# Kernel optimization log

Measured on AMD Instinct MI355X. Metric: run time of the kernel, lower is better.

Reference implementation:

```python
import jax, jax.numpy as jnp
import numpy as np

B, S, D = 4, 2048, 1024
H, HD = 16, 64

def setup_inputs() -> dict:
    key = jax.random.key(0)
    ks = jax.random.split(key, 5)
    scale = 1.0 / np.sqrt(D)
    return {
        "x": jax.random.normal(ks[0], (B, S, D), dtype=jnp.float32),
        "Wq": jax.random.normal(ks[1], (D, D), dtype=jnp.float32) * scale,
        "Wk": jax.random.normal(ks[2], (D, D), dtype=jnp.float32) * scale,
        "Wv": jax.random.normal(ks[3], (D, D), dtype=jnp.float32) * scale,
        "Wo": jax.random.normal(ks[4], (D, D), dtype=jnp.float32) * scale,
        "bo": jnp.zeros((D,), dtype=jnp.float32),
    }

def reference(x, Wq, Wk, Wv, Wo, bo):
    batch, tokens, _ = x.shape
    # Linear weights applied as x @ W^T to match torch nn.Linear; here W is [out,in] equiv square
    q = (x @ Wq).reshape(batch, tokens, H, HD).transpose(0, 2, 1, 3)  # [B,H,S,HD]
    k = (x @ Wk).reshape(batch, tokens, H, HD).transpose(0, 2, 1, 3)
    v = (x @ Wv).reshape(batch, tokens, H, HD).transpose(0, 2, 1, 3)
    scores = jnp.einsum('bhqd,bhkd->bhqk', q, k) / jnp.sqrt(jnp.float32(HD))
    causal = jnp.tril(jnp.ones((tokens, tokens), dtype=bool))  # True = keep
    scores = jnp.where(causal[None, None], scores, -jnp.inf)
    attn = jax.nn.softmax(scores, axis=-1)  # dropout is identity (eval / rate 0)
    ctx = jnp.einsum('bhqk,bhkd->bhqd', attn, v)
    ctx = ctx.transpose(0, 2, 1, 3).reshape(batch, tokens, D)
    return ctx @ Wo + bo
```

## Files before the change

kernel.cpp:

```cpp
#include <hip/hip_runtime.h>
#include <math.h>
#include <stdint.h>

constexpr int kB = 4;
constexpr int kS = 2048;
constexpr int kD = 1024;
constexpr int kH = 16;
constexpr int kHD = 64;

typedef __bf16 bf16;
typedef __attribute__((ext_vector_type(4))) __bf16 bf16x4;
typedef __attribute__((ext_vector_type(8))) __bf16 bf16x8;
typedef __attribute__((ext_vector_type(4))) float f32x4;

__device__ __forceinline__ f32x4 mfma16x16x32(bf16x8 a, bf16x8 b, f32x4 c) {
    return __builtin_amdgcn_mfma_f32_16x16x32_bf16(a, b, c, 0, 0, 0);
}

#if __has_builtin(__builtin_amdgcn_exp2f)
#define EXP2F(x) __builtin_amdgcn_exp2f(x)
#else
#define EXP2F(x) exp2f(x)
#endif

__device__ __forceinline__ void load_lds16(const bf16* g, bf16* lds) {
    __builtin_amdgcn_global_load_lds(
        (const __attribute__((address_space(1))) void*)g,
        (__attribute__((address_space(3))) void*)lds, 16, 0, 0);
}

__global__ __launch_bounds__(256) void prep_x(const float* __restrict__ x,
                                              bf16* __restrict__ xb) {
    size_t i = ((size_t)blockIdx.x * 256 + threadIdx.x) * 8;
    float4 f0 = *(const float4*)(x + i);
    float4 f1 = *(const float4*)(x + i + 4);
    bf16x8 v;
    v[0] = (bf16)f0.x; v[1] = (bf16)f0.y; v[2] = (bf16)f0.z; v[3] = (bf16)f0.w;
    v[4] = (bf16)f1.x; v[5] = (bf16)f1.y; v[6] = (bf16)f1.z; v[7] = (bf16)f1.w;
    *(bf16x8*)(xb + i) = v;
}

__global__ __launch_bounds__(256) void prep_w(const float* __restrict__ Wq,
                                              const float* __restrict__ Wk,
                                              const float* __restrict__ Wv,
                                              const float* __restrict__ Wo,
                                              bf16* __restrict__ Wt) {
    __shared__ bf16 t[64 * 72];
    const int z = blockIdx.z;
    const float* W = (z == 0) ? Wq : (z == 1) ? Wk : (z == 2) ? Wv : Wo;
    const float scale = (z == 0) ? 0.18033688011112042f : 1.0f;
    const int k0 = blockIdx.x * 64, n0 = blockIdx.y * 64;
    const int tid = threadIdx.x;
    for (int p = 0; p < 16; ++p) {
        int idx = tid + p * 256;
        int r = idx >> 6, c = idx & 63;
        t[r * 72 + c] = (bf16)(W[(size_t)(k0 + r) * kD + n0 + c] * scale);
    }
    __syncthreads();
    for (int p = 0; p < 16; ++p) {
        int idx = tid + p * 256;
        int r = idx >> 6, c = idx & 63;
        Wt[(size_t)(z * 1024 + n0 + r) * kD + k0 + c] = t[c * 72 + r];
    }
}

__global__ __launch_bounds__(256) void qkv_gemm(
    const bf16* __restrict__ xb, const bf16* __restrict__ Wt,
    bf16* __restrict__ qo, bf16* __restrict__ ko, bf16* __restrict__ vto)
{
    __shared__ bf16 As[128 * 32];
    __shared__ bf16 Bs[128 * 32];

    const int tid  = threadIdx.x;
    const int wave = tid >> 6;
    const int lane = tid & 63;
    const int quad = lane >> 4;
    const int lr   = lane & 15;
    const int wm   = wave >> 1, wn = wave & 1;

    const int m0 = blockIdx.x * 128;
    const int n0 = blockIdx.y * 128;

    const int sr = tid >> 2, sc = tid & 3;

    f32x4 acc[4][4];
#pragma unroll
    for (int i = 0; i < 4; ++i)
#pragma unroll
        for (int nt = 0; nt < 4; ++nt) acc[i][nt] = f32x4{0.f, 0.f, 0.f, 0.f};

    for (int k0 = 0; k0 < kD; k0 += 32) {
        __syncthreads();
#pragma unroll
        for (int p = 0; p < 2; ++p) {
            int r = p * 64 + sr;
            load_lds16(&xb[(size_t)(m0 + r) * kD + k0 + sc * 8],
                       &As[(p * 256 + wave * 64) * 8]);
            load_lds16(&Wt[(size_t)(n0 + r) * kD + k0 + sc * 8],
                       &Bs[(p * 256 + wave * 64) * 8]);
        }
        __syncthreads();
        bf16x8 a[4], b[4];
#pragma unroll
        for (int i = 0; i < 4; ++i)
            a[i] = *(const bf16x8*)&As[(wm * 64 + i * 16 + lr) * 32 + quad * 8];
#pragma unroll
        for (int nt = 0; nt < 4; ++nt)
            b[nt] = *(const bf16x8*)&Bs[(wn * 64 + nt * 16 + lr) * 32 + quad * 8];
#pragma unroll
        for (int i = 0; i < 4; ++i)
#pragma unroll
            for (int nt = 0; nt < 4; ++nt)
                acc[i][nt] = mfma16x16x32(a[i], b[nt], acc[i][nt]);
    }

    const int w_idx = n0 >> 10;
    if (w_idx < 2) {
        bf16* dst = (w_idx == 0) ? qo : ko;
#pragma unroll
        for (int i = 0; i < 4; ++i)
#pragma unroll
            for (int nt = 0; nt < 4; ++nt) {
                int n   = n0 + wn * 64 + nt * 16 + lr;
                int col = n & 1023;
#pragma unroll
                for (int j = 0; j < 4; ++j) {
                    int m = m0 + wm * 64 + i * 16 + quad * 4 + j;
                    dst[(size_t)m * kD + col] = (bf16)acc[i][nt][j];
                }
            }
    } else {
#pragma unroll
        for (int i = 0; i < 4; ++i)
#pragma unroll
            for (int nt = 0; nt < 4; ++nt) {
                int n   = n0 + wn * 64 + nt * 16 + lr;
                int col = n & 1023, h = col >> 6, hd = col & 63;
                int mb  = m0 + wm * 64 + i * 16 + quad * 4;
                int b = mb >> 11, s = mb & 2047;
                bf16x4 pk;
#pragma unroll
                for (int j = 0; j < 4; ++j) pk[j] = (bf16)acc[i][nt][j];
                *(bf16x4*)&vto[((size_t)(b * kH + h) * kHD + hd) * kS + s] = pk;
            }
    }
}

__global__ __launch_bounds__(256, 3) void attn(
    const bf16* __restrict__ q, const bf16* __restrict__ k,
    const bf16* __restrict__ vt, bf16* __restrict__ ctx)
{
    __shared__ bf16 Ks[2][64 * 64];
    __shared__ bf16 Vs[2][64 * 64];
    __shared__ bf16 Pl[4][16 * 72];

    const int tid  = threadIdx.x;
    const int wave = tid >> 6;
    const int lane = tid & 63;
    const int quad = lane >> 4;
    const int lr   = lane & 15;

    const int bh = blockIdx.x;
    const int qb = gridDim.y - 1 - blockIdx.y;
    const int b  = bh >> 4;
    const int h  = bh & 15;

    const bf16* qb_p = q  + (size_t)b * kS * kD + h * kHD;
    const bf16* kb_p = k  + (size_t)b * kS * kD + h * kHD;
    const bf16* vt_p = vt + (size_t)bh * kHD * kS;

    const int T    = qb + 1;
    const int base = qb * 64 + wave * 16;

    const int grow   = lane >> 3;
    const int gchunk = ((lane & 7) ^ (grow & 7)) * 8;

    bf16x8 ones;
#pragma unroll
    for (int i = 0; i < 8; ++i) ones[i] = (bf16)1.0f;

    bf16x8 aq[2];
#pragma unroll
    for (int kk = 0; kk < 2; ++kk)
        aq[kk] = *(const bf16x8*)&qb_p[(size_t)(base + lr) * kD + kk * 32 + quad * 8];

    f32x4 o[4];
    f32x4 lacc = f32x4{0.f, 0.f, 0.f, 0.f};
#pragma unroll
    for (int nt = 0; nt < 4; ++nt) o[nt] = f32x4{0.f, 0.f, 0.f, 0.f};

    bf16* Pw = &Pl[wave][0];

    if (wave == 0) {
#pragma unroll
        for (int i = 0; i < 8; ++i)
            load_lds16(kb_p + (size_t)(i * 8 + grow) * kD + gchunk, &Ks[0][i * 512]);
    } else if (wave == 1) {
#pragma unroll
        for (int i = 0; i < 8; ++i)
            load_lds16(vt_p + (size_t)(i * 8 + grow) * kS + gchunk, &Vs[0][i * 512]);
    }
    __syncthreads();

#pragma unroll 1
    for (int kt = 0; kt < T; ++kt) {
        const int k0  = kt * 64;
        const int buf = kt & 1;

        if (kt + 1 < T) {
            const int nk0 = k0 + 64;
            if (wave == 0) {
#pragma unroll
                for (int i = 0; i < 8; ++i)
                    load_lds16(kb_p + (size_t)(nk0 + i * 8 + grow) * kD + gchunk,
                               &Ks[buf ^ 1][i * 512]);
            } else if (wave == 1) {
#pragma unroll
                for (int i = 0; i < 8; ++i)
                    load_lds16(vt_p + (size_t)(i * 8 + grow) * kS + nk0 + gchunk,
                               &Vs[buf ^ 1][i * 512]);
            }
        }

        bf16x8 kf[4][2], vf[4][2];
#pragma unroll
        for (int nt = 0; nt < 4; ++nt)
#pragma unroll
            for (int kk = 0; kk < 2; ++kk) {
                const int sw = ((kk * 4 + quad) ^ (lr & 7)) << 3;
                kf[nt][kk] = *(const bf16x8*)&Ks[buf][(nt * 16 + lr) * 64 + sw];
                vf[nt][kk] = *(const bf16x8*)&Vs[buf][(nt * 16 + lr) * 64 + sw];
            }

        f32x4 sg[4];
        __builtin_amdgcn_s_setprio(1);
#pragma unroll
        for (int nt = 0; nt < 4; ++nt) {
            sg[nt] = mfma16x16x32(kf[nt][0], aq[0], f32x4{0.f, 0.f, 0.f, 0.f});
            sg[nt] = mfma16x16x32(kf[nt][1], aq[1], sg[nt]);
        }
        __builtin_amdgcn_s_setprio(0);

        if (kt == T - 1) {
            const int qg = base + lr;
#pragma unroll
            for (int nt = 0; nt < 4; ++nt) {
                bf16x4 pk;
#pragma unroll
                for (int j = 0; j < 4; ++j) {
                    float s = sg[nt][j];
                    s = (k0 + nt * 16 + quad * 4 + j > qg) ? -3.0e38f : s;
                    pk[j] = (bf16)EXP2F(s);
                }
                *(bf16x4*)&Pw[lr * 72 + nt * 16 + quad * 4] = pk;
            }
        } else {
#pragma unroll
            for (int nt = 0; nt < 4; ++nt) {
                bf16x4 pk;
#pragma unroll
                for (int j = 0; j < 4; ++j) pk[j] = (bf16)EXP2F(sg[nt][j]);
                *(bf16x4*)&Pw[lr * 72 + nt * 16 + quad * 4] = pk;
            }
        }

        __builtin_amdgcn_s_setprio(1);
#pragma unroll
        for (int kk = 0; kk < 2; ++kk) {
            bf16x8 pa = *(const bf16x8*)&Pw[lr * 72 + kk * 32 + quad * 8];
            lacc = mfma16x16x32(pa, ones, lacc);
#pragma unroll
            for (int nt = 0; nt < 4; ++nt)
                o[nt] = mfma16x16x32(pa, vf[nt][kk], o[nt]);
        }
        __builtin_amdgcn_s_setprio(0);

        __syncthreads();
    }

    float inv[4];
#pragma unroll
    for (int j = 0; j < 4; ++j) inv[j] = 1.0f / lacc[j];
#pragma unroll
    for (int nt = 0; nt < 4; ++nt) {
        int hd = nt * 16 + lr;
#pragma unroll
        for (int j = 0; j < 4; ++j) {
            int qg = base + quad * 4 + j;
            ctx[((size_t)(b * kS + qg)) * kD + h * kHD + hd] = (bf16)(o[nt][j] * inv[j]);
        }
    }
}

__global__ __launch_bounds__(256) void out_gemm(
    const bf16* __restrict__ ctxb, const bf16* __restrict__ Wto,
    const float* __restrict__ bo, float* __restrict__ out)
{
    __shared__ bf16 As[128 * 32];
    __shared__ bf16 Bs[128 * 32];

    const int tid  = threadIdx.x;
    const int wave = tid >> 6;
    const int lane = tid & 63;
    const int quad = lane >> 4;
    const int lr   = lane & 15;
    const int wm   = wave >> 1, wn = wave & 1;

    const int m0 = blockIdx.x * 128;
    const int n0 = blockIdx.y * 128;

    const int sr = tid >> 2, sc = tid & 3;

    f32x4 acc[4][4];
#pragma unroll
    for (int i = 0; i < 4; ++i)
#pragma unroll
        for (int nt = 0; nt < 4; ++nt) acc[i][nt] = f32x4{0.f, 0.f, 0.f, 0.f};

    for (int k0 = 0; k0 < kD; k0 += 32) {
        __syncthreads();
#pragma unroll
        for (int p = 0; p < 2; ++p) {
            int r = p * 64 + sr;
            load_lds16(&ctxb[(size_t)(m0 + r) * kD + k0 + sc * 8],
                       &As[(p * 256 + wave * 64) * 8]);
            load_lds16(&Wto[(size_t)(n0 + r) * kD + k0 + sc * 8],
                       &Bs[(p * 256 + wave * 64) * 8]);
        }
        __syncthreads();
        bf16x8 a[4], b[4];
#pragma unroll
        for (int i = 0; i < 4; ++i)
            a[i] = *(const bf16x8*)&As[(wm * 64 + i * 16 + lr) * 32 + quad * 8];
#pragma unroll
        for (int nt = 0; nt < 4; ++nt)
            b[nt] = *(const bf16x8*)&Bs[(wn * 64 + nt * 16 + lr) * 32 + quad * 8];
#pragma unroll
        for (int i = 0; i < 4; ++i)
#pragma unroll
            for (int nt = 0; nt < 4; ++nt)
                acc[i][nt] = mfma16x16x32(a[i], b[nt], acc[i][nt]);
    }

#pragma unroll
    for (int nt = 0; nt < 4; ++nt) {
        int n = n0 + wn * 64 + nt * 16 + lr;
        float bias = bo[n];
#pragma unroll
        for (int i = 0; i < 4; ++i)
#pragma unroll
            for (int j = 0; j < 4; ++j) {
                int m = m0 + wm * 64 + i * 16 + quad * 4 + j;
                out[(size_t)m * kD + n] = acc[i][nt][j] + bias;
            }
    }
}

extern "C" void kernel_launch(void* const* d_in, const int* in_sizes, int n_in,
                              void* d_out, int out_size, void* d_ws, size_t ws_size,
                              hipStream_t stream) {
    const float* x  = (const float*)d_in[0];
    const float* Wq = (const float*)d_in[1];
    const float* Wk = (const float*)d_in[2];
    const float* Wv = (const float*)d_in[3];
    const float* Wo = (const float*)d_in[4];
    const float* bo = (const float*)d_in[5];
    float* out = (float*)d_out;

    const size_t n_x   = (size_t)kB * kS * kD;
    const size_t n_w   = (size_t)4 * kD * kD;
    const size_t n_mat = (size_t)kB * kH * kS * kHD;

    bf16* xb  = (bf16*)d_ws;
    bf16* Wt  = xb + n_x;
    bf16* Qm  = Wt + n_w;
    bf16* Km  = Qm + n_mat;
    bf16* Vt  = Km + n_mat;
    bf16* ctx = xb;

    prep_x<<<dim3((int)(n_x / (256 * 8))), dim3(256), 0, stream>>>(x, xb);
    prep_w<<<dim3(16, 16, 4), dim3(256), 0, stream>>>(Wq, Wk, Wv, Wo, Wt);
    qkv_gemm<<<dim3(8192 / 128, 3072 / 128), dim3(256), 0, stream>>>(xb, Wt, Qm, Km, Vt);
    attn<<<dim3(kB * kH, 32), dim3(256), 0, stream>>>(Qm, Km, Vt, ctx);
    out_gemm<<<dim3(8192 / 128, 1024 / 128), dim3(256), 0, stream>>>(
        ctx, Wt + (size_t)3 * kD * kD, bo, out);
}
```

Baseline: 239.9 us.

## Double-buffer LDS tiles in QKV and output GEMMs with prefetch and setprio

Both projection GEMMs now hold two LDS buffers per operand. The next K-slice is issued as a direct global-to-LDS load while the current slice's MFMAs run, and the loop drops from two barriers per iteration to one. The MFMA block is wrapped in s_setprio to favour matrix issue. This doubles LDS use per block, which may lower occupancy, and correctness relies on the vmcnt wait that the single barrier implies for the async LDS loads.

```diff
diff --git a/kernel.cpp b/kernel.cpp
--- a/kernel.cpp
+++ b/kernel.cpp
@@ -68,8 +68,8 @@
     const bf16* __restrict__ xb, const bf16* __restrict__ Wt,
     bf16* __restrict__ qo, bf16* __restrict__ ko, bf16* __restrict__ vto)
 {
-    __shared__ bf16 As[128 * 32];
-    __shared__ bf16 Bs[128 * 32];
+    __shared__ bf16 As[2][128 * 32];
+    __shared__ bf16 Bs[2][128 * 32];
 
     const int tid  = threadIdx.x;
     const int wave = tid >> 6;
@@ -89,29 +89,44 @@
 #pragma unroll
         for (int nt = 0; nt < 4; ++nt) acc[i][nt] = f32x4{0.f, 0.f, 0.f, 0.f};
 
+#pragma unroll
+    for (int p = 0; p < 2; ++p) {
+        int r = p * 64 + sr;
+        load_lds16(&xb[(size_t)(m0 + r) * kD + sc * 8], &As[0][(p * 256 + wave * 64) * 8]);
+        load_lds16(&Wt[(size_t)(n0 + r) * kD + sc * 8], &Bs[0][(p * 256 + wave * 64) * 8]);
+    }
+    __syncthreads();
+
+    int buf = 0;
     for (int k0 = 0; k0 < kD; k0 += 32) {
-        __syncthreads();
-#pragma unroll
-        for (int p = 0; p < 2; ++p) {
-            int r = p * 64 + sr;
-            load_lds16(&xb[(size_t)(m0 + r) * kD + k0 + sc * 8],
-                       &As[(p * 256 + wave * 64) * 8]);
-            load_lds16(&Wt[(size_t)(n0 + r) * kD + k0 + sc * 8],
-                       &Bs[(p * 256 + wave * 64) * 8]);
-        }
-        __syncthreads();
+        if (k0 + 32 < kD) {
+#pragma unroll
+            for (int p = 0; p < 2; ++p) {
+                int r = p * 64 + sr;
+                load_lds16(&xb[(size_t)(m0 + r) * kD + k0 + 32 + sc * 8],
+                           &As[buf ^ 1][(p * 256 + wave * 64) * 8]);
+                load_lds16(&Wt[(size_t)(n0 + r) * kD + k0 + 32 + sc * 8],
+                           &Bs[buf ^ 1][(p * 256 + wave * 64) * 8]);
+            }
+        }
+
         bf16x8 a[4], b[4];
 #pragma unroll
         for (int i = 0; i < 4; ++i)
-            a[i] = *(const bf16x8*)&As[(wm * 64 + i * 16 + lr) * 32 + quad * 8];
+            a[i] = *(const bf16x8*)&As[buf][(wm * 64 + i * 16 + lr) * 32 + quad * 8];
 #pragma unroll
         for (int nt = 0; nt < 4; ++nt)
-            b[nt] = *(const bf16x8*)&Bs[(wn * 64 + nt * 16 + lr) * 32 + quad * 8];
+            b[nt] = *(const bf16x8*)&Bs[buf][(wn * 64 + nt * 16 + lr) * 32 + quad * 8];
+        __builtin_amdgcn_s_setprio(1);
 #pragma unroll
         for (int i = 0; i < 4; ++i)
 #pragma unroll
             for (int nt = 0; nt < 4; ++nt)
                 acc[i][nt] = mfma16x16x32(a[i], b[nt], acc[i][nt]);
+        __builtin_amdgcn_s_setprio(0);
+
+        __syncthreads();
+        buf ^= 1;
     }
 
     const int w_idx = n0 >> 10;
@@ -296,8 +311,8 @@
     const bf16* __restrict__ ctxb, const bf16* __restrict__ Wto,
     const float* __restrict__ bo, float* __restrict__ out)
 {
-    __shared__ bf16 As[128 * 32];
-    __shared__ bf16 Bs[128 * 32];
+    __shared__ bf16 As[2][128 * 32];
+    __shared__ bf16 Bs[2][128 * 32];
 
     const int tid  = threadIdx.x;
     const int wave = tid >> 6;
@@ -317,29 +332,44 @@
 #pragma unroll
         for (int nt = 0; nt < 4; ++nt) acc[i][nt] = f32x4{0.f, 0.f, 0.f, 0.f};
 
+#pragma unroll
+    for (int p = 0; p < 2; ++p) {
+        int r = p * 64 + sr;
+        load_lds16(&ctxb[(size_t)(m0 + r) * kD + sc * 8], &As[0][(p * 256 + wave * 64) * 8]);
+        load_lds16(&Wto[(size_t)(n0 + r) * kD + sc * 8], &Bs[0][(p * 256 + wave * 64) * 8]);
+    }
+    __syncthreads();
+
+    int buf = 0;
     for (int k0 = 0; k0 < kD; k0 += 32) {
-        __syncthreads();
-#pragma unroll
-        for (int p = 0; p < 2; ++p) {
-            int r = p * 64 + sr;
-            load_lds16(&ctxb[(size_t)(m0 + r) * kD + k0 + sc * 8],
-                       &As[(p * 256 + wave * 64) * 8]);
-            load_lds16(&Wto[(size_t)(n0 + r) * kD + k0 + sc * 8],
-                       &Bs[(p * 256 + wave * 64) * 8]);
-        }
-        __syncthreads();
+        if (k0 + 32 < kD) {
+#pragma unroll
+            for (int p = 0; p < 2; ++p) {
+                int r = p * 64 + sr;
+                load_lds16(&ctxb[(size_t)(m0 + r) * kD + k0 + 32 + sc * 8],
+                           &As[buf ^ 1][(p * 256 + wave * 64) * 8]);
+                load_lds16(&Wto[(size_t)(n0 + r) * kD + k0 + 32 + sc * 8],
+                           &Bs[buf ^ 1][(p * 256 + wave * 64) * 8]);
+            }
+        }
+
         bf16x8 a[4], b[4];
 #pragma unroll
         for (int i = 0; i < 4; ++i)
-            a[i] = *(const bf16x8*)&As[(wm * 64 + i * 16 + lr) * 32 + quad * 8];
+            a[i] = *(const bf16x8*)&As[buf][(wm * 64 + i * 16 + lr) * 32 + quad * 8];
 #pragma unroll
         for (int nt = 0; nt < 4; ++nt)
-            b[nt] = *(const bf16x8*)&Bs[(wn * 64 + nt * 16 + lr) * 32 + quad * 8];
+            b[nt] = *(const bf16x8*)&Bs[buf][(wn * 64 + nt * 16 + lr) * 32 + quad * 8];
+        __builtin_amdgcn_s_setprio(1);
 #pragma unroll
         for (int i = 0; i < 4; ++i)
 #pragma unroll
             for (int nt = 0; nt < 4; ++nt)
                 acc[i][nt] = mfma16x16x32(a[i], b[nt], acc[i][nt]);
+        __builtin_amdgcn_s_setprio(0);
+
+        __syncthreads();
+        buf ^= 1;
     }
 
 #pragma unroll
```

Result: slower. 245.5 us (+2.3%).

## Rewrite QKV GEMM with 256x256 tiles, double-buffered LDS and XOR swizzle

Applied to the files above, without the earlier changes.

The QKV projection GEMM moves from 128x128 tiles with 256 threads and a synchronous K=32 loop to 256x256 tiles with 512 threads and K=64 steps. Global-to-LDS loads are double-buffered and interleaved with MFMA phases using explicit barriers, waitcnt and setprio, and LDS reads use an XOR swizzle to avoid bank conflicts. The aim is to hide memory latency and raise data reuse per tile. In exchange it needs 128KB of LDS and many more accumulator registers, which limits occupancy and leaves only 384 blocks across the grid.

```diff
diff --git a/kernel.cpp b/kernel.cpp
--- a/kernel.cpp
+++ b/kernel.cpp
@@ -64,86 +64,146 @@
     }
 }
 
-__global__ __launch_bounds__(256) void qkv_gemm(
+__global__ __launch_bounds__(512) void qkv_gemm(
     const bf16* __restrict__ xb, const bf16* __restrict__ Wt,
     bf16* __restrict__ qo, bf16* __restrict__ ko, bf16* __restrict__ vto)
 {
-    __shared__ bf16 As[128 * 32];
-    __shared__ bf16 Bs[128 * 32];
+    __shared__ bf16 As[2][256 * 64];
+    __shared__ bf16 Bs[2][256 * 64];
 
     const int tid  = threadIdx.x;
     const int wave = tid >> 6;
     const int lane = tid & 63;
     const int quad = lane >> 4;
     const int lr   = lane & 15;
-    const int wm   = wave >> 1, wn = wave & 1;
-
-    const int m0 = blockIdx.x * 128;
-    const int n0 = blockIdx.y * 128;
-
-    const int sr = tid >> 2, sc = tid & 3;
-
-    f32x4 acc[4][4];
-#pragma unroll
-    for (int i = 0; i < 4; ++i)
+    const int wm   = wave >> 2;
+    const int wn   = wave & 3;
+
+    const int m0 = blockIdx.x * 256;
+    const int n0 = blockIdx.y * 256;
+
+    const int srow   = tid >> 3;
+    const int schunk = ((tid & 7) ^ ((tid >> 3) & 7)) * 8;
+
+#define STG_A(b_, kt_, h_) do {                                                \
+    const int ktc = (kt_) < 16 ? (kt_) : 15;                                   \
+    const size_t kc = (size_t)ktc * 64 + schunk;                               \
+    load_lds16(&xb[(size_t)(m0 + (h_)*128 +      srow) * kD + kc],             \
+               &As[b_][((h_)*128 +      wave * 8) * 64]);                      \
+    load_lds16(&xb[(size_t)(m0 + (h_)*128 + 64 + srow) * kD + kc],             \
+               &As[b_][((h_)*128 + 64 + wave * 8) * 64]);                      \
+  } while (0)
+#define STG_B(b_, kt_, h_) do {                                                \
+    const int ktc = (kt_) < 16 ? (kt_) : 15;                                   \
+    const size_t kc = (size_t)ktc * 64 + schunk;                               \
+    load_lds16(&Wt[(size_t)(n0 + (h_)*128 +      srow) * kD + kc],             \
+               &Bs[b_][((h_)*128 +      wave * 8) * 64]);                      \
+    load_lds16(&Wt[(size_t)(n0 + (h_)*128 + 64 + srow) * kD + kc],             \
+               &Bs[b_][((h_)*128 + 64 + wave * 8) * 64]);                      \
+  } while (0)
+
+#define READ_A(B_, I_, KK_) \
+    (*(const bf16x8*)&As[B_][(wm * 128 + (I_)*16 + lr) * 64 + ((((KK_)*4 + quad) ^ (lr & 7)) << 3)])
+#define READ_B(B_, NT_, KK_) \
+    (*(const bf16x8*)&Bs[B_][(wn * 64 + (NT_)*16 + lr) * 64 + ((((KK_)*4 + quad) ^ (lr & 7)) << 3)])
+
+#define PH(B_, I0_, RB_, STMT, DOVM) do {                                      \
+    bf16x8 a00 = READ_A(B_, I0_, 0);                                           \
+    bf16x8 a01 = READ_A(B_, I0_, 1);                                           \
+    bf16x8 a10 = READ_A(B_, (I0_) + 1, 0);                                     \
+    bf16x8 a11 = READ_A(B_, (I0_) + 1, 1);                                     \
+    if (RB_) {                                                                 \
+        _Pragma("unroll")                                                      \
+        for (int nt = 0; nt < 4; ++nt) {                                       \
+            br[nt][0] = READ_B(B_, nt, 0);                                     \
+            br[nt][1] = READ_B(B_, nt, 1);                                     \
+        }                                                                      \
+    }                                                                          \
+    STMT;                                                                      \
+    __builtin_amdgcn_s_barrier();                                              \
+    asm volatile("s_waitcnt lgkmcnt(0)" ::: "memory");                         \
+    __builtin_amdgcn_sched_barrier(0);                                         \
+    __builtin_amdgcn_s_setprio(1);                                             \
+    _Pragma("unroll")                                                          \
+    for (int nt = 0; nt < 4; ++nt) {                                           \
+        acc[I0_][nt]       = mfma16x16x32(a00, br[nt][0], acc[I0_][nt]);       \
+        acc[I0_][nt]       = mfma16x16x32(a01, br[nt][1], acc[I0_][nt]);       \
+        acc[(I0_) + 1][nt] = mfma16x16x32(a10, br[nt][0], acc[(I0_) + 1][nt]); \
+        acc[(I0_) + 1][nt] = mfma16x16x32(a11, br[nt][1], acc[(I0_) + 1][nt]); \
+    }                                                                          \
+    __builtin_amdgcn_s_setprio(0);                                             \
+    if (DOVM) {                                                                \
+        asm volatile("s_waitcnt vmcnt(4)" ::: "memory");                       \
+        __builtin_amdgcn_sched_barrier(0);                                     \
+    }                                                                          \
+    __builtin_amdgcn_s_barrier();                                              \
+  } while (0)
+
+    f32x4 acc[8][4];
+#pragma unroll
+    for (int i = 0; i < 8; ++i)
 #pragma unroll
         for (int nt = 0; nt < 4; ++nt) acc[i][nt] = f32x4{0.f, 0.f, 0.f, 0.f};
 
-    for (int k0 = 0; k0 < kD; k0 += 32) {
-        __syncthreads();
-#pragma unroll
-        for (int p = 0; p < 2; ++p) {
-            int r = p * 64 + sr;
-            load_lds16(&xb[(size_t)(m0 + r) * kD + k0 + sc * 8],
-                       &As[(p * 256 + wave * 64) * 8]);
-            load_lds16(&Wt[(size_t)(n0 + r) * kD + k0 + sc * 8],
-                       &Bs[(p * 256 + wave * 64) * 8]);
-        }
-        __syncthreads();
-        bf16x8 a[4], b[4];
-#pragma unroll
-        for (int i = 0; i < 4; ++i)
-            a[i] = *(const bf16x8*)&As[(wm * 64 + i * 16 + lr) * 32 + quad * 8];
-#pragma unroll
-        for (int nt = 0; nt < 4; ++nt)
-            b[nt] = *(const bf16x8*)&Bs[(wn * 64 + nt * 16 + lr) * 32 + quad * 8];
-#pragma unroll
-        for (int i = 0; i < 4; ++i)
-#pragma unroll
-            for (int nt = 0; nt < 4; ++nt)
-                acc[i][nt] = mfma16x16x32(a[i], b[nt], acc[i][nt]);
+    bf16x8 br[4][2];
+
+    STG_B(0, 0, 0); STG_B(0, 0, 1);
+    STG_A(0, 0, 0); STG_A(0, 0, 1);
+    STG_B(1, 1, 0); STG_B(1, 1, 1);
+    asm volatile("s_waitcnt vmcnt(4)" ::: "memory");
+    __builtin_amdgcn_sched_barrier(0);
+    __builtin_amdgcn_s_barrier();
+
+#pragma unroll 1
+    for (int j = 0; j < 8; ++j) {
+        const int t1  = 2 * j + 1;
+        const int tn0 = 2 * j + 2;
+        const int tn1 = 2 * j + 3;
+        PH(0, 0, 1, STG_A(1, t1, 0),  0);
+        PH(0, 2, 0, STG_A(1, t1, 1),  0);
+        PH(0, 4, 0, STG_B(0, tn0, 0), 0);
+        PH(0, 6, 0, STG_B(0, tn0, 1), 1);
+        PH(1, 0, 1, STG_A(0, tn0, 0), 0);
+        PH(1, 2, 0, STG_A(0, tn0, 1), 0);
+        PH(1, 4, 0, STG_B(1, tn1, 0), 0);
+        PH(1, 6, 0, STG_B(1, tn1, 1), 1);
     }
 
     const int w_idx = n0 >> 10;
     if (w_idx < 2) {
         bf16* dst = (w_idx == 0) ? qo : ko;
 #pragma unroll
-        for (int i = 0; i < 4; ++i)
+        for (int i = 0; i < 8; ++i)
 #pragma unroll
             for (int nt = 0; nt < 4; ++nt) {
                 int n   = n0 + wn * 64 + nt * 16 + lr;
                 int col = n & 1023;
 #pragma unroll
-                for (int j = 0; j < 4; ++j) {
-                    int m = m0 + wm * 64 + i * 16 + quad * 4 + j;
-                    dst[(size_t)m * kD + col] = (bf16)acc[i][nt][j];
+                for (int jj = 0; jj < 4; ++jj) {
+                    int m = m0 + wm * 128 + i * 16 + quad * 4 + jj;
+                    dst[(size_t)m * kD + col] = (bf16)acc[i][nt][jj];
                 }
             }
     } else {
 #pragma unroll
-        for (int i = 0; i < 4; ++i)
+        for (int i = 0; i < 8; ++i)
 #pragma unroll
             for (int nt = 0; nt < 4; ++nt) {
                 int n   = n0 + wn * 64 + nt * 16 + lr;
                 int col = n & 1023, h = col >> 6, hd = col & 63;
-                int mb  = m0 + wm * 64 + i * 16 + quad * 4;
+                int mb  = m0 + wm * 128 + i * 16 + quad * 4;
                 int b = mb >> 11, s = mb & 2047;
                 bf16x4 pk;
 #pragma unroll
-                for (int j = 0; j < 4; ++j) pk[j] = (bf16)acc[i][nt][j];
+                for (int jj = 0; jj < 4; ++jj) pk[jj] = (bf16)acc[i][nt][jj];
                 *(bf16x4*)&vto[((size_t)(b * kH + h) * kHD + hd) * kS + s] = pk;
             }
     }
+#undef PH
+#undef READ_A
+#undef READ_B
+#undef STG_A
+#undef STG_B
 }
 
 __global__ __launch_bounds__(256, 3) void attn(
@@ -380,7 +440,7 @@
 
     prep_x<<<dim3((int)(n_x / (256 * 8))), dim3(256), 0, stream>>>(x, xb);
     prep_w<<<dim3(16, 16, 4), dim3(256), 0, stream>>>(Wq, Wk, Wv, Wo, Wt);
-    qkv_gemm<<<dim3(8192 / 128, 3072 / 128), dim3(256), 0, stream>>>(xb, Wt, Qm, Km, Vt);
+    qkv_gemm<<<dim3(8192 / 256, 3072 / 256), dim3(512), 0, stream>>>(xb, Wt, Qm, Km, Vt);
     attn<<<dim3(kB * kH, 32), dim3(256), 0, stream>>>(Qm, Km, Vt, ctx);
     out_gemm<<<dim3(8192 / 128, 1024 / 128), dim3(256), 0, stream>>>(
         ctx, Wt + (size_t)3 * kD * kD, bo, out);
```

New measurement: 243.3 us. Within noise of the previous version (+1.4%).
